# Optimization experiments

Hardware: AMD Instinct MI355X
Metric: run time of the kernel (lower is better)

## Reference

```python
import jax, jax.numpy as jnp
import numpy as np

N = 50000   # nodes
E = 600000  # edges per relation
F = 256     # dim_features
H = 128     # dim_hiddens == dim_embs
Q = 64      # dim_query
R = 2       # relations per sign (etypes)
L = 2       # conv_depth


def setup_inputs() -> dict:
    key = jax.random.key(0)
    ks = jax.random.split(key, 11)
    s = 0.05
    return {
        "x_attr": jax.random.normal(ks[0], (N, F), jnp.float32),
        "x_stru": jax.random.normal(ks[1], (N, F), jnp.float32),
        # edges_*: [sign(pos/neg), relation, (src,dst), E]
        "edges_attr": jax.random.randint(ks[2], (2, R, 2, E), 0, N),
        "edges_stru": jax.random.randint(ks[3], (2, R, 2, E), 0, N),
        # params, leading dim 2 = (pos_emb_model, neg_emb_model)
        "Wf": jax.random.normal(ks[4], (2, H, F), jnp.float32) * s,
        "convW": jax.random.normal(ks[5], (2, L, R, H, H), jnp.float32) * s,
        "convB": jnp.zeros((2, L, R, H), jnp.float32),
        "attnW1": jax.random.normal(ks[6], (2, L, H, Q), jnp.float32) * s,
        "attnB1": jnp.zeros((2, L, Q), jnp.float32),
        "attnW2": jax.random.normal(ks[7], (2, L, Q), jnp.float32) * s,
        "Wc": jax.random.normal(ks[8], (2, H, 3 * H), jnp.float32) * s,
    }


def _gcn(h, src, dst, W, b):
    """DGL GraphConv, norm='both', degrees clamped to >=1."""
    n = h.shape[0]
    ones = jnp.ones(src.shape[0], h.dtype)
    deg_out = jnp.clip(jax.ops.segment_sum(ones, src, num_segments=n), 1.0)
    deg_in = jnp.clip(jax.ops.segment_sum(ones, dst, num_segments=n), 1.0)
    m = (h * (deg_out ** -0.5)[:, None]) @ W          # (N, H)
    agg = jax.ops.segment_sum(m[src], dst, num_segments=n)  # gather-scatter over edges
    return agg * (deg_in ** -0.5)[:, None] + b


def _het_layer(h, edges, Ws, bs, W1, b1, w2):
    """HeteroGraphConv with per-node attention aggregation over relations.
    edges: (R, 2, E); Ws: (R,H,H); bs: (R,H)."""
    hs = jnp.stack([_gcn(h, edges[r, 0], edges[r, 1], Ws[r], bs[r]) for r in range(R)])  # (R,N,H)
    scores = jnp.einsum('rnq,q->rn', jnp.tanh(jnp.einsum('rnd,dq->rnq', hs, W1) + b1), w2)
    a = jax.nn.softmax(scores, axis=0)                # (R,N) attention over relations
    return jnp.einsum('rn,rnd->nd', a, hs), a


def _hetattn(x, edges, Wf, cW, cB, aW1, aB1, aW2, Wc):
    h0 = jnp.tanh(x @ Wf.T)                                        # (N,H)
    h1, _ = _het_layer(h0, edges, cW[1], cB[1], aW1[1], aB1[1], aW2[1])   # 1-hop via last conv
    hA, _ = _het_layer(h0, edges, cW[0], cB[0], aW1[0], aB1[0], aW2[0])
    h2, attn = _het_layer(hA, edges, cW[1], cB[1], aW1[1], aB1[1], aW2[1])  # 2-hop
    y = jnp.concatenate([h0, h1, h2], axis=-1) @ Wc.T              # concat_weight
    return y, attn.T


def reference(x_attr, x_stru, edges_attr, edges_stru, Wf, convW, convB,
              attnW1, attnB1, attnW2, Wc):
    def run(sign, x, edges):
        y, _ = _hetattn(x, edges[sign], Wf[sign], convW[sign], convB[sign],
                        attnW1[sign], attnB1[sign], attnW2[sign], Wc[sign])
        return y
    embs_attr_pos = run(0, x_attr, edges_attr)
    embs_stru_pos = run(0, x_stru, edges_stru)
    embs_attr_neg = run(1, x_attr, edges_attr)
    embs_stru_neg = run(1, x_stru, edges_stru)
    return (embs_attr_pos, embs_stru_pos, embs_attr_neg, embs_stru_neg)
```

## Files before the change

### kernel.cpp

```cpp
#include <hip/hip_runtime.h>
#include <math.h>

constexpr int N_ = 50000;
constexpr int E_ = 600000;
constexpr int F_ = 256;
constexpr int H_ = 128;
constexpr int Q_ = 64;
constexpr int R_ = 2;
constexpr int L_ = 2;

#define MODE_STORE 0
#define MODE_TANH  1
#define MODE_ACC   2

template <bool BT>
__global__ __launch_bounds__(256) void gemm_kernel(
    const float* __restrict__ A, int lda,
    const float* __restrict__ B, int ldb,
    float* __restrict__ C, int ldc,
    int M, int K,
    const float* __restrict__ rowscale, int mode)
{
    __shared__ __align__(16) float As[16][68];
    __shared__ __align__(16) float Bs[16][68];

    const int row0 = blockIdx.x * 64;
    const int col0 = blockIdx.y * 64;
    const int tid  = threadIdx.x;
    const int tm = tid >> 4;
    const int tn = tid & 15;

    float acc[4][4] = {};

    for (int kk = 0; kk < K; kk += 16) {
        {
            const int m  = tid >> 2;
            const int k4 = (tid & 3) * 4;
            const int r  = row0 + m;
            float4 v = make_float4(0.f, 0.f, 0.f, 0.f);
            if (r < M) v = *(const float4*)(A + (size_t)r * lda + kk + k4);
            As[k4 + 0][m] = v.x; As[k4 + 1][m] = v.y;
            As[k4 + 2][m] = v.z; As[k4 + 3][m] = v.w;
        }
        if (BT) {
            const int j  = tid >> 2;
            const int k4 = (tid & 3) * 4;
            float4 v = *(const float4*)(B + (size_t)(col0 + j) * ldb + kk + k4);
            Bs[k4 + 0][j] = v.x; Bs[k4 + 1][j] = v.y;
            Bs[k4 + 2][j] = v.z; Bs[k4 + 3][j] = v.w;
        } else {
            const int k  = tid >> 4;
            const int j4 = (tid & 15) * 4;
            float4 v = *(const float4*)(B + (size_t)(kk + k) * ldb + col0 + j4);
            Bs[k][j4 + 0] = v.x; Bs[k][j4 + 1] = v.y;
            Bs[k][j4 + 2] = v.z; Bs[k][j4 + 3] = v.w;
        }
        __syncthreads();

        #pragma unroll
        for (int k = 0; k < 16; k++) {
            const float4 av = *(const float4*)&As[k][tm * 4];
            const float4 bv = *(const float4*)&Bs[k][tn * 4];
            const float a[4] = {av.x, av.y, av.z, av.w};
            const float b[4] = {bv.x, bv.y, bv.z, bv.w};
            #pragma unroll
            for (int i = 0; i < 4; i++)
                #pragma unroll
                for (int j = 0; j < 4; j++)
                    acc[i][j] += a[i] * b[j];
        }
        __syncthreads();
    }

    #pragma unroll
    for (int i = 0; i < 4; i++) {
        const int r = row0 + tm * 4 + i;
        if (r >= M) continue;
        const float rs = rowscale ? rowscale[r] : 1.0f;
        #pragma unroll
        for (int j = 0; j < 4; j++) {
            const int c = col0 + tn * 4 + j;
            float v = acc[i][j] * rs;
            if (mode == MODE_TANH) v = tanhf(v);
            float* p = C + (size_t)r * ldc + c;
            if (mode == MODE_ACC) *p += v;
            else                  *p = v;
        }
    }
}

__global__ __launch_bounds__(256) void gemm_conv_pair(
    const float* __restrict__ A, int lda,
    const float* __restrict__ B0, const float* __restrict__ B1,
    float* __restrict__ C0, float* __restrict__ C1,
    int M, const float* __restrict__ rs0, const float* __restrict__ rs1)
{
    __shared__ __align__(16) float As[16][68];
    __shared__ __align__(16) float B0s[16][68];
    __shared__ __align__(16) float B1s[16][68];

    const int row0 = blockIdx.x * 64;
    const int col0 = blockIdx.y * 64;
    const int tid  = threadIdx.x;
    const int tm = tid >> 4;
    const int tn = tid & 15;

    float acc0[4][4] = {};
    float acc1[4][4] = {};

    for (int kk = 0; kk < H_; kk += 16) {
        {
            const int m  = tid >> 2;
            const int k4 = (tid & 3) * 4;
            const int r  = row0 + m;
            float4 v = make_float4(0.f, 0.f, 0.f, 0.f);
            if (r < M) v = *(const float4*)(A + (size_t)r * lda + kk + k4);
            As[k4 + 0][m] = v.x; As[k4 + 1][m] = v.y;
            As[k4 + 2][m] = v.z; As[k4 + 3][m] = v.w;
        }
        {
            const int k  = tid >> 4;
            const int j4 = (tid & 15) * 4;
            float4 v0 = *(const float4*)(B0 + (size_t)(kk + k) * H_ + col0 + j4);
            float4 v1 = *(const float4*)(B1 + (size_t)(kk + k) * H_ + col0 + j4);
            B0s[k][j4 + 0] = v0.x; B0s[k][j4 + 1] = v0.y;
            B0s[k][j4 + 2] = v0.z; B0s[k][j4 + 3] = v0.w;
            B1s[k][j4 + 0] = v1.x; B1s[k][j4 + 1] = v1.y;
            B1s[k][j4 + 2] = v1.z; B1s[k][j4 + 3] = v1.w;
        }
        __syncthreads();

        #pragma unroll
        for (int k = 0; k < 16; k++) {
            const float4 av  = *(const float4*)&As[k][tm * 4];
            const float4 bv0 = *(const float4*)&B0s[k][tn * 4];
            const float4 bv1 = *(const float4*)&B1s[k][tn * 4];
            const float a[4]  = {av.x, av.y, av.z, av.w};
            const float b0[4] = {bv0.x, bv0.y, bv0.z, bv0.w};
            const float b1v[4] = {bv1.x, bv1.y, bv1.z, bv1.w};
            #pragma unroll
            for (int i = 0; i < 4; i++)
                #pragma unroll
                for (int j = 0; j < 4; j++) {
                    acc0[i][j] += a[i] * b0[j];
                    acc1[i][j] += a[i] * b1v[j];
                }
        }
        __syncthreads();
    }

    #pragma unroll
    for (int i = 0; i < 4; i++) {
        const int r = row0 + tm * 4 + i;
        if (r >= M) continue;
        const float s0 = rs0[r];
        const float s1 = rs1[r];
        #pragma unroll
        for (int j = 0; j < 4; j++) {
            const int c = col0 + tn * 4 + j;
            C0[(size_t)r * H_ + c] = acc0[i][j] * s0;
            C1[(size_t)r * H_ + c] = acc1[i][j] * s1;
        }
    }
}

__global__ __launch_bounds__(256) void zero_i(int* __restrict__ p, int n)
{
    int t = blockIdx.x * 256 + threadIdx.x;
    if (t < n) p[t] = 0;
}

__global__ __launch_bounds__(256) void count_deg(const int* __restrict__ eb,
                                                 int* __restrict__ cnt, int total)
{
    int t = blockIdx.x * 256 + threadIdx.x;
    if (t >= total) return;
    int which = t / E_;
    atomicAdd(&cnt[which * N_ + eb[t]], 1);
}

__global__ __launch_bounds__(256) void deg_finalize(const int* __restrict__ cnt,
                                                    float* __restrict__ dscale, int n)
{
    int t = blockIdx.x * 256 + threadIdx.x;
    if (t < n) {
        int v = cnt[t];
        dscale[t] = rsqrtf((float)(v < 1 ? 1 : v));
    }
}

__global__ __launch_bounds__(1024) void scan_offs(const int* __restrict__ cnt,
                                                  int* __restrict__ offs,
                                                  int* __restrict__ cursor)
{
    __shared__ int part[1024];
    const int r = blockIdx.x;
    const int* in = cnt + (size_t)(2 * r + 1) * N_;
    int* out = offs + (size_t)r * (N_ + 1);
    int* cur = cursor + (size_t)r * N_;

    constexpr int CH = (N_ + 1023) / 1024;
    const int lo = threadIdx.x * CH;
    const int hi = (lo + CH < N_) ? lo + CH : N_;

    int s = 0;
    for (int i = lo; i < hi; i++) s += in[i];
    part[threadIdx.x] = s;
    __syncthreads();

    #pragma unroll
    for (int d = 1; d < 1024; d <<= 1) {
        int t = (threadIdx.x >= d) ? part[threadIdx.x - d] : 0;
        __syncthreads();
        part[threadIdx.x] += t;
        __syncthreads();
    }

    int run = part[threadIdx.x] - s;
    for (int i = lo; i < hi; i++) {
        int v = in[i];
        out[i] = run;
        cur[i] = run;
        run += v;
    }
    if (threadIdx.x == 1023) out[N_] = run;
}

__global__ __launch_bounds__(256) void csr_fill(const int* __restrict__ eb,
                                                int* __restrict__ cursor,
                                                int* __restrict__ csr, int total)
{
    int t = blockIdx.x * 256 + threadIdx.x;
    if (t >= total) return;
    int r = (t >= E_) ? 1 : 0;
    int e = t - r * E_;
    int s = eb[(r * 2 + 0) * E_ + e];
    int d = eb[(r * 2 + 1) * E_ + e];
    int pos = atomicAdd(&cursor[r * N_ + d], 1);
    csr[(size_t)r * E_ + pos] = s;
}

__device__ __forceinline__ void gather_rel(const float2* __restrict__ m,
                                           const int* __restrict__ csr,
                                           int b, int e, int lane, float2& acc)
{
    int k = b;
    for (; k + 4 <= e; k += 4) {
        const int s0 = csr[k + 0];
        const int s1 = csr[k + 1];
        const int s2 = csr[k + 2];
        const int s3 = csr[k + 3];
        const float2 v0 = m[(size_t)s0 * 64 + lane];
        const float2 v1 = m[(size_t)s1 * 64 + lane];
        const float2 v2 = m[(size_t)s2 * 64 + lane];
        const float2 v3 = m[(size_t)s3 * 64 + lane];
        acc.x += (v0.x + v1.x) + (v2.x + v3.x);
        acc.y += (v0.y + v1.y) + (v2.y + v3.y);
    }
    for (; k < e; k++) {
        const int s = csr[k];
        const float2 v = m[(size_t)s * 64 + lane];
        acc.x += v.x; acc.y += v.y;
    }
}

__global__ __launch_bounds__(1024, 8) void pull_attn(
    const float2* __restrict__ m0, const float2* __restrict__ m1,
    const int* __restrict__ offs0, const int* __restrict__ csr0,
    const int* __restrict__ offs1, const int* __restrict__ csr1,
    const float* __restrict__ si0, const float* __restrict__ si1,
    const float* __restrict__ bias0, const float* __restrict__ bias1,
    const float* __restrict__ W1, const float* __restrict__ b1,
    const float* __restrict__ w2, float2* __restrict__ outb, int n)
{
    __shared__ float W1s[H_ * Q_];
    __shared__ float2 hsS[16][2][Q_];
    __shared__ float b1s[Q_], w2s[Q_], bAs[H_], bBs[H_];

    for (int i = threadIdx.x; i < H_ * Q_; i += 1024) W1s[i] = W1[i];
    if (threadIdx.x < Q_) { b1s[threadIdx.x] = b1[threadIdx.x]; w2s[threadIdx.x] = w2[threadIdx.x]; }
    {
        const int t = (int)threadIdx.x - Q_;
        if (t >= 0 && t < H_) bAs[t] = bias0[t];
        const int u = (int)threadIdx.x - Q_ - H_;
        if (u >= 0 && u < H_) bBs[u] = bias1[u];
    }
    __syncthreads();

    const int lane = threadIdx.x & 63;
    const int wv   = threadIdx.x >> 6;
    int node = (blockIdx.x * 1024 + threadIdx.x) >> 6;
    node = __builtin_amdgcn_readfirstlane(node);

    float2 hs0 = make_float2(0.f, 0.f), hs1 = hs0;

    if (node < n) {
        float2 a0 = make_float2(0.f, 0.f), a1 = a0;
        const int b0  = offs0[node], e0 = offs0[node + 1];
        const int b1i = offs1[node], e1 = offs1[node + 1];
        gather_rel(m0, csr0, b0,  e0, lane, a0);
        gather_rel(m1, csr1, b1i, e1, lane, a1);

        const float sc0 = si0[node], sc1 = si1[node];
        hs0.x = a0.x * sc0 + bAs[2 * lane];
        hs0.y = a0.y * sc0 + bAs[2 * lane + 1];
        hs1.x = a1.x * sc1 + bBs[2 * lane];
        hs1.y = a1.y * sc1 + bBs[2 * lane + 1];
        hsS[wv][0][lane] = hs0;
        hsS[wv][1][lane] = hs1;
    }

    __asm__ volatile("s_waitcnt lgkmcnt(0)" ::: "memory");
    __builtin_amdgcn_sched_barrier(0);

    if (node < n) {
        const float* h0p = (const float*)&hsS[wv][0][0];
        const float* h1p = (const float*)&hsS[wv][1][0];
        float t0 = b1s[lane], t1 = b1s[lane];
        #pragma unroll 8
        for (int i = 0; i < H_; i++) {
            const float wval = W1s[i * Q_ + lane];
            t0 += h0p[i] * wval;
            t1 += h1p[i] * wval;
        }
        float s0 = tanhf(t0) * w2s[lane];
        float s1 = tanhf(t1) * w2s[lane];
        #pragma unroll
        for (int off = 32; off > 0; off >>= 1) {
            s0 += __shfl_xor(s0, off);
            s1 += __shfl_xor(s1, off);
        }
        const float mx = fmaxf(s0, s1);
        const float e0v = expf(s0 - mx), e1v = expf(s1 - mx);
        const float a0 = e0v / (e0v + e1v), a1 = 1.0f - a0;

        float2 o;
        o.x = a0 * hs0.x + a1 * hs1.x;
        o.y = a0 * hs0.y + a1 * hs1.y;
        outb[(size_t)node * 64 + lane] = o;
    }
}

extern "C" void kernel_launch(void* const* d_in, const int* in_sizes, int n_in,
                              void* d_out, int out_size, void* d_ws, size_t ws_size,
                              hipStream_t stream)
{
    const float* x_attr = (const float*)d_in[0];
    const float* x_stru = (const float*)d_in[1];
    const int*   e_attr = (const int*)d_in[2];
    const int*   e_stru = (const int*)d_in[3];
    const float* Wf     = (const float*)d_in[4];
    const float* convW  = (const float*)d_in[5];
    const float* convB  = (const float*)d_in[6];
    const float* aW1    = (const float*)d_in[7];
    const float* aB1    = (const float*)d_in[8];
    const float* aW2    = (const float*)d_in[9];
    const float* Wc     = (const float*)d_in[10];
    float*       out    = (float*)d_out;
    float*       ws     = (float*)d_ws;

    const size_t NH = (size_t)N_ * H_;
    float* A  = ws;
    float* Bb = ws + 1 * NH;
    float* C  = ws + 2 * NH;
    float* D  = ws + 3 * NH;
    float* dscale = ws + 4 * NH;
    int*   ibase  = (int*)(dscale + 4 * N_);
    int*   cnt    = ibase;
    int*   offs   = ibase + 4 * N_;
    int*   csr    = offs + 2 * (N_ + 1);
    int*   cursor = csr + 2 * E_;

    const int GX = (N_ + 63) / 64;
    const dim3 GGRID(GX, 2);
    const int PA_B = (N_ * 64) / 1024;

    for (int run = 0; run < 4; run++) {
        const int sign = run >> 1;
        const float* x = (run & 1) ? x_stru : x_attr;
        const int* eb = ((run & 1) ? e_stru : e_attr) + (size_t)sign * (R_ * 2 * E_);
        float* y = out + (size_t)run * NH;
        const float* WcS = Wc + (size_t)sign * H_ * 3 * H_;

        zero_i<<<(4 * N_ + 255) / 256, 256, 0, stream>>>(cnt, 4 * N_);
        count_deg<<<(4 * E_ + 255) / 256, 256, 0, stream>>>(eb, cnt, 4 * E_);
        deg_finalize<<<(4 * N_ + 255) / 256, 256, 0, stream>>>(cnt, dscale, 4 * N_);
        scan_offs<<<2, 1024, 0, stream>>>(cnt, offs, cursor);
        csr_fill<<<(2 * E_ + 255) / 256, 256, 0, stream>>>(eb, cursor, csr, 2 * E_);

        gemm_kernel<true><<<GGRID, 256, 0, stream>>>(
            x, F_, Wf + (size_t)sign * H_ * F_, F_, A, H_, N_, F_, nullptr, MODE_TANH);

        gemm_kernel<true><<<GGRID, 256, 0, stream>>>(
            A, H_, WcS, 3 * H_, y, H_, N_, H_, nullptr, MODE_STORE);

        auto het = [&](const float* h_in, int l, float* outb) {
            const size_t lo = (size_t)(sign * L_ + l);
            gemm_conv_pair<<<GGRID, 256, 0, stream>>>(
                h_in, H_,
                convW + (lo * R_ + 0) * H_ * H_,
                convW + (lo * R_ + 1) * H_ * H_,
                C, D, N_,
                dscale + 0 * N_, dscale + 2 * N_);
            pull_attn<<<PA_B, 1024, 0, stream>>>(
                (const float2*)C, (const float2*)D,
                offs, csr, offs + (N_ + 1), csr + E_,
                dscale + N_, dscale + 3 * N_,
                convB + (lo * R_ + 0) * H_, convB + (lo * R_ + 1) * H_,
                aW1 + lo * H_ * Q_, aB1 + lo * Q_, aW2 + lo * Q_,
                (float2*)outb, N_);
        };

        het(A, 1, Bb);
        gemm_kernel<true><<<GGRID, 256, 0, stream>>>(
            Bb, H_, WcS + H_, 3 * H_, y, H_, N_, H_, nullptr, MODE_ACC);

        het(A, 0, Bb);

        het(Bb, 1, A);
        gemm_kernel<true><<<GGRID, 256, 0, stream>>>(
            A, H_, WcS + 2 * H_, 3 * H_, y, H_, N_, H_, nullptr, MODE_ACC);
    }
}
```

Before: 3.886 ms.

## Widen GEMM tile to 128 columns, parallelize scan, deepen gather unroll

The generic GEMM now computes 64x128 tiles with an 8-column per-thread accumulator, so A is loaded once per block instead of twice. The single-block-per-relation 1024-thread scan is replaced by a three-phase multi-block scan that spreads the prefix sum across many workgroups. The edge gather loop is unrolled to 8 independent loads to raise memory-level parallelism. The changes raise register use in the GEMM and add two kernel launches per run.

```diff
diff --git a/kernel.cpp b/kernel.cpp
--- a/kernel.cpp
+++ b/kernel.cpp
@@ -22,15 +22,15 @@
     const float* __restrict__ rowscale, int mode)
 {
     __shared__ __align__(16) float As[16][68];
-    __shared__ __align__(16) float Bs[16][68];
+    __shared__ __align__(16) float Bs[16][132];
 
     const int row0 = blockIdx.x * 64;
-    const int col0 = blockIdx.y * 64;
+    const int col0 = blockIdx.y * 128;
     const int tid  = threadIdx.x;
     const int tm = tid >> 4;
     const int tn = tid & 15;
 
-    float acc[4][4] = {};
+    float acc[4][8] = {};
 
     for (int kk = 0; kk < K; kk += 16) {
         {
@@ -43,30 +43,39 @@
             As[k4 + 2][m] = v.z; As[k4 + 3][m] = v.w;
         }
         if (BT) {
-            const int j  = tid >> 2;
-            const int k4 = (tid & 3) * 4;
-            float4 v = *(const float4*)(B + (size_t)(col0 + j) * ldb + kk + k4);
-            Bs[k4 + 0][j] = v.x; Bs[k4 + 1][j] = v.y;
-            Bs[k4 + 2][j] = v.z; Bs[k4 + 3][j] = v.w;
+            const int j  = tid >> 1;
+            const int k8 = (tid & 1) * 8;
+            const float* bp = B + (size_t)(col0 + j) * ldb + kk + k8;
+            float4 v0 = *(const float4*)(bp);
+            float4 v1 = *(const float4*)(bp + 4);
+            Bs[k8 + 0][j] = v0.x; Bs[k8 + 1][j] = v0.y;
+            Bs[k8 + 2][j] = v0.z; Bs[k8 + 3][j] = v0.w;
+            Bs[k8 + 4][j] = v1.x; Bs[k8 + 5][j] = v1.y;
+            Bs[k8 + 6][j] = v1.z; Bs[k8 + 7][j] = v1.w;
         } else {
-            const int k  = tid >> 4;
-            const int j4 = (tid & 15) * 4;
-            float4 v = *(const float4*)(B + (size_t)(kk + k) * ldb + col0 + j4);
-            Bs[k][j4 + 0] = v.x; Bs[k][j4 + 1] = v.y;
-            Bs[k][j4 + 2] = v.z; Bs[k][j4 + 3] = v.w;
+            const int k  = tid >> 5;
+            const int j4 = (tid & 31) * 4;
+            float4 v0 = *(const float4*)(B + (size_t)(kk + k) * ldb + col0 + j4);
+            float4 v1 = *(const float4*)(B + (size_t)(kk + k + 8) * ldb + col0 + j4);
+            Bs[k + 0][j4 + 0] = v0.x; Bs[k + 0][j4 + 1] = v0.y;
+            Bs[k + 0][j4 + 2] = v0.z; Bs[k + 0][j4 + 3] = v0.w;
+            Bs[k + 8][j4 + 0] = v1.x; Bs[k + 8][j4 + 1] = v1.y;
+            Bs[k + 8][j4 + 2] = v1.z; Bs[k + 8][j4 + 3] = v1.w;
         }
         __syncthreads();
 
         #pragma unroll
         for (int k = 0; k < 16; k++) {
-            const float4 av = *(const float4*)&As[k][tm * 4];
-            const float4 bv = *(const float4*)&Bs[k][tn * 4];
+            const float4 av  = *(const float4*)&As[k][tm * 4];
+            const float4 bv0 = *(const float4*)&Bs[k][tn * 8];
+            const float4 bv1 = *(const float4*)&Bs[k][tn * 8 + 4];
             const float a[4] = {av.x, av.y, av.z, av.w};
-            const float b[4] = {bv.x, bv.y, bv.z, bv.w};
+            const float b[8] = {bv0.x, bv0.y, bv0.z, bv0.w,
+                                bv1.x, bv1.y, bv1.z, bv1.w};
             #pragma unroll
             for (int i = 0; i < 4; i++)
                 #pragma unroll
-                for (int j = 0; j < 4; j++)
+                for (int j = 0; j < 8; j++)
                     acc[i][j] += a[i] * b[j];
         }
         __syncthreads();
@@ -78,8 +87,8 @@
         if (r >= M) continue;
         const float rs = rowscale ? rowscale[r] : 1.0f;
         #pragma unroll
-        for (int j = 0; j < 4; j++) {
-            const int c = col0 + tn * 4 + j;
+        for (int j = 0; j < 8; j++) {
+            const int c = col0 + tn * 8 + j;
             float v = acc[i][j] * rs;
             if (mode == MODE_TANH) v = tanhf(v);
             float* p = C + (size_t)r * ldc + c;
@@ -189,41 +198,67 @@
     }
 }
 
-__global__ __launch_bounds__(1024) void scan_offs(const int* __restrict__ cnt,
-                                                  int* __restrict__ offs,
-                                                  int* __restrict__ cursor)
-{
-    __shared__ int part[1024];
+constexpr int SCAN_NB = (N_ + 255) / 256;
+
+__global__ __launch_bounds__(256) void scan_p1(const int* __restrict__ cnt,
+                                               int* __restrict__ bsums)
+{
+    const int r = blockIdx.y;
+    const int* in = cnt + (size_t)(2 * r + 1) * N_;
+    const int i = blockIdx.x * 256 + threadIdx.x;
+    int v = (i < N_) ? in[i] : 0;
+    #pragma unroll
+    for (int off = 32; off > 0; off >>= 1) v += __shfl_xor(v, off);
+    __shared__ int ws[4];
+    if ((threadIdx.x & 63) == 0) ws[threadIdx.x >> 6] = v;
+    __syncthreads();
+    if (threadIdx.x == 0)
+        bsums[r * SCAN_NB + blockIdx.x] = ws[0] + ws[1] + ws[2] + ws[3];
+}
+
+__global__ __launch_bounds__(256) void scan_p2(int* __restrict__ bsums)
+{
+    __shared__ int sh[256];
     const int r = blockIdx.x;
+    const int t = threadIdx.x;
+    int v = (t < SCAN_NB) ? bsums[r * SCAN_NB + t] : 0;
+    sh[t] = v;
+    __syncthreads();
+    #pragma unroll
+    for (int d = 1; d < 256; d <<= 1) {
+        int u = (t >= d) ? sh[t - d] : 0;
+        __syncthreads();
+        sh[t] += u;
+        __syncthreads();
+    }
+    if (t < SCAN_NB) bsums[r * SCAN_NB + t] = sh[t] - v;
+}
+
+__global__ __launch_bounds__(256) void scan_p3(const int* __restrict__ cnt,
+                                               const int* __restrict__ bsums,
+                                               int* __restrict__ offs,
+                                               int* __restrict__ cursor)
+{
+    __shared__ int sh[256];
+    const int r = blockIdx.y;
     const int* in = cnt + (size_t)(2 * r + 1) * N_;
     int* out = offs + (size_t)r * (N_ + 1);
     int* cur = cursor + (size_t)r * N_;
-
-    constexpr int CH = (N_ + 1023) / 1024;
-    const int lo = threadIdx.x * CH;
-    const int hi = (lo + CH < N_) ? lo + CH : N_;
-
-    int s = 0;
-    for (int i = lo; i < hi; i++) s += in[i];
-    part[threadIdx.x] = s;
+    const int i = blockIdx.x * 256 + threadIdx.x;
+    const int t = threadIdx.x;
+    int v = (i < N_) ? in[i] : 0;
+    sh[t] = v;
     __syncthreads();
-
     #pragma unroll
-    for (int d = 1; d < 1024; d <<= 1) {
-        int t = (threadIdx.x >= d) ? part[threadIdx.x - d] : 0;
-        __syncthreads();
-        part[threadIdx.x] += t;
-        __syncthreads();
-    }
-
-    int run = part[threadIdx.x] - s;
-    for (int i = lo; i < hi; i++) {
-        int v = in[i];
-        out[i] = run;
-        cur[i] = run;
-        run += v;
-    }
-    if (threadIdx.x == 1023) out[N_] = run;
+    for (int d = 1; d < 256; d <<= 1) {
+        int u = (t >= d) ? sh[t - d] : 0;
+        __syncthreads();
+        sh[t] += u;
+        __syncthreads();
+    }
+    const int excl = sh[t] - v + bsums[r * SCAN_NB + blockIdx.x];
+    if (i < N_) { out[i] = excl; cur[i] = excl; }
+    if (i == 0) out[N_] = E_;
 }
 
 __global__ __launch_bounds__(256) void csr_fill(const int* __restrict__ eb,
@@ -245,7 +280,17 @@
                                            int b, int e, int lane, float2& acc)
 {
     int k = b;
-    for (; k + 4 <= e; k += 4) {
+    for (; k + 8 <= e; k += 8) {
+        int s[8];
+        #pragma unroll
+        for (int u = 0; u < 8; u++) s[u] = csr[k + u];
+        float2 v[8];
+        #pragma unroll
+        for (int u = 0; u < 8; u++) v[u] = m[(size_t)s[u] * 64 + lane];
+        #pragma unroll
+        for (int u = 0; u < 8; u++) { acc.x += v[u].x; acc.y += v[u].y; }
+    }
+    if (k + 4 <= e) {
         const int s0 = csr[k + 0];
         const int s1 = csr[k + 1];
         const int s2 = csr[k + 2];
@@ -256,6 +301,7 @@
         const float2 v3 = m[(size_t)s3 * 64 + lane];
         acc.x += (v0.x + v1.x) + (v2.x + v3.x);
         acc.y += (v0.y + v1.y) + (v2.y + v3.y);
+        k += 4;
     }
     for (; k < e; k++) {
         const int s = csr[k];
@@ -370,9 +416,12 @@
     int*   offs   = ibase + 4 * N_;
     int*   csr    = offs + 2 * (N_ + 1);
     int*   cursor = csr + 2 * E_;
+    int*   bsums  = cursor + 2 * N_;
 
     const int GX = (N_ + 63) / 64;
-    const dim3 GGRID(GX, 2);
+    const dim3 GGEMM(GX, 1);
+    const dim3 GCONV(GX, 2);
+    const dim3 GSCAN(SCAN_NB, 2);
     const int PA_B = (N_ * 64) / 1024;
 
     for (int run = 0; run < 4; run++) {
@@ -385,18 +434,20 @@
         zero_i<<<(4 * N_ + 255) / 256, 256, 0, stream>>>(cnt, 4 * N_);
         count_deg<<<(4 * E_ + 255) / 256, 256, 0, stream>>>(eb, cnt, 4 * E_);
         deg_finalize<<<(4 * N_ + 255) / 256, 256, 0, stream>>>(cnt, dscale, 4 * N_);
-        scan_offs<<<2, 1024, 0, stream>>>(cnt, offs, cursor);
+        scan_p1<<<GSCAN, 256, 0, stream>>>(cnt, bsums);
+        scan_p2<<<2, 256, 0, stream>>>(bsums);
+        scan_p3<<<GSCAN, 256, 0, stream>>>(cnt, bsums, offs, cursor);
         csr_fill<<<(2 * E_ + 255) / 256, 256, 0, stream>>>(eb, cursor, csr, 2 * E_);
 
-        gemm_kernel<true><<<GGRID, 256, 0, stream>>>(
+        gemm_kernel<true><<<GGEMM, 256, 0, stream>>>(
             x, F_, Wf + (size_t)sign * H_ * F_, F_, A, H_, N_, F_, nullptr, MODE_TANH);
 
-        gemm_kernel<true><<<GGRID, 256, 0, stream>>>(
+        gemm_kernel<true><<<GGEMM, 256, 0, stream>>>(
             A, H_, WcS, 3 * H_, y, H_, N_, H_, nullptr, MODE_STORE);
 
         auto het = [&](const float* h_in, int l, float* outb) {
             const size_t lo = (size_t)(sign * L_ + l);
-            gemm_conv_pair<<<GGRID, 256, 0, stream>>>(
+            gemm_conv_pair<<<GCONV, 256, 0, stream>>>(
                 h_in, H_,
                 convW + (lo * R_ + 0) * H_ * H_,
                 convW + (lo * R_ + 1) * H_ * H_,
@@ -412,13 +463,13 @@
         };
 
         het(A, 1, Bb);
-        gemm_kernel<true><<<GGRID, 256, 0, stream>>>(
+        gemm_kernel<true><<<GGEMM, 256, 0, stream>>>(
             Bb, H_, WcS + H_, 3 * H_, y, H_, N_, H_, nullptr, MODE_ACC);
 
         het(A, 0, Bb);
 
         het(Bb, 1, A);
-        gemm_kernel<true><<<GGRID, 256, 0, stream>>>(
+        gemm_kernel<true><<<GGEMM, 256, 0, stream>>>(
             A, H_, WcS + 2 * H_, 3 * H_, y, H_, N_, H_, nullptr, MODE_ACC);
     }
 }
```

New measurement: 3.660 ms. -5.8%, faster.
